# Kernel optimization log

Measured on AMD Instinct MI355X. Metric: run time of the kernel, lower is better.

Reference implementation:

```python
import jax, jax.numpy as jnp
import numpy as np

N_HEADS = 16
D_K = 64  # d_model / n_heads = 1024 / 16


def setup_inputs() -> dict:
    key = jax.random.key(0)
    ks = jax.random.split(key, 7)
    B, S, D = 4, 2048, 1024
    scale = 1.0 / np.sqrt(D)
    return {
        "Q": jax.random.normal(ks[0], (B, S, D), dtype=jnp.float32),
        "K": jax.random.normal(ks[1], (B, S, D), dtype=jnp.float32),
        "V": jax.random.normal(ks[2], (B, S, D), dtype=jnp.float32),
        # Linear weights stored as [in, out] so y = x @ W (bias=False in original).
        "WQ": jax.random.normal(ks[3], (D, D), dtype=jnp.float32) * scale,
        "WK": jax.random.normal(ks[4], (D, D), dtype=jnp.float32) * scale,
        "WV": jax.random.normal(ks[5], (D, D), dtype=jnp.float32) * scale,
        "Wfc": jax.random.normal(ks[6], (D, D), dtype=jnp.float32) * scale,
    }


def reference(Q, K, V, WQ, WK, WV, Wfc):
    B = Q.shape[0]
    # NOTE: the original uses a raw reshape [B, S, H*dk] -> [B, H, S, dk]
    # (NOT the usual view+transpose); row-major reshape reproduces it exactly.
    q = (Q @ WQ).reshape(B, N_HEADS, -1, D_K)  # [B, H, S, dk]
    k = (K @ WK).reshape(B, N_HEADS, -1, D_K)
    v = (V @ WV).reshape(B, N_HEADS, -1, D_K)
    scores = jnp.einsum("bhqd,bhkd->bhqk", q, k) / jnp.sqrt(jnp.asarray(D_K, q.dtype))
    attn = jax.nn.softmax(scores, axis=-1)
    ctx = jnp.einsum("bhqk,bhkd->bhqd", attn, v)  # [B, H, S, dk]
    ctx = jnp.transpose(ctx, (0, 2, 1, 3)).reshape(B, -1, N_HEADS * D_K)  # [B, S, D]
    return ctx @ Wfc
```

## Files before the change

### kernel.cpp

```cpp
#include <hip/hip_runtime.h>
#include <stdint.h>
#include <math.h>


typedef __attribute__((ext_vector_type(8))) short short8;
typedef __attribute__((ext_vector_type(4))) float f32x4;
typedef __attribute__((ext_vector_type(16))) float f32x16;
typedef __attribute__((ext_vector_type(2))) unsigned int u32x2;
typedef __attribute__((ext_vector_type(4))) unsigned int u32x4;
typedef __attribute__((ext_vector_type(8))) _Float16 half8;

__device__ __forceinline__ unsigned short bf16rne(float f) {
  unsigned int u = __builtin_bit_cast(unsigned int, f);
  unsigned int r = u + 0x7FFFu + ((u >> 16) & 1u);
  return (unsigned short)(r >> 16);
}

__device__ __forceinline__ void gld_lds16(const void* g, void* l) {
  typedef __attribute__((address_space(3))) unsigned int lds_u32;
  typedef const __attribute__((address_space(1))) unsigned int glb_u32;
  __builtin_amdgcn_global_load_lds((glb_u32*)(uintptr_t)g,
                                   (lds_u32*)(unsigned int)(uintptr_t)l,
                                   16, 0, 0);
}

__device__ __forceinline__ unsigned pkrtz(float a, float b) {
  auto h = __builtin_amdgcn_cvt_pkrtz(a, b);
  return __builtin_bit_cast(unsigned, h);
}

__device__ __forceinline__ float fexp2(float x) {
#if __has_builtin(__builtin_amdgcn_exp2f)
  return __builtin_amdgcn_exp2f(x);
#else
  float r;
  asm("v_exp_f32 %0, %1" : "=v"(r) : "v"(x));
  return r;
#endif
}

__device__ __forceinline__ float max3f(float a, float b, float c) {
  float r;
  asm("v_max3_f32 %0, %1, %2, %3" : "=v"(r) : "v"(a), "v"(b), "v"(c));
  return r;
}

__global__ void convert_x_kernel(const float* __restrict__ Q,
                                 const float* __restrict__ K,
                                 const float* __restrict__ V,
                                 unsigned short* __restrict__ Xb) {
  const int z = blockIdx.y;
  const float* src = (z == 0) ? Q : (z == 1) ? K : V;
  const size_t i0 = ((size_t)blockIdx.x * 256 + threadIdx.x) * 8;
  const f32x4 a = *(const f32x4*)(src + i0);
  const f32x4 c = *(const f32x4*)(src + i0 + 4);
  u32x4 o;
  o[0] = (unsigned)bf16rne(a[0]) | ((unsigned)bf16rne(a[1]) << 16);
  o[1] = (unsigned)bf16rne(a[2]) | ((unsigned)bf16rne(a[3]) << 16);
  o[2] = (unsigned)bf16rne(c[0]) | ((unsigned)bf16rne(c[1]) << 16);
  o[3] = (unsigned)bf16rne(c[2]) | ((unsigned)bf16rne(c[3]) << 16);
  *(u32x4*)(Xb + (size_t)z * 8388608 + i0) = o;
}

__global__ void convert_w_kernel(const float* __restrict__ W0,
                                 const float* __restrict__ W1,
                                 const float* __restrict__ W2,
                                 const float* __restrict__ W3,
                                 unsigned short* __restrict__ Wt) {
  const int z = blockIdx.z;
  const float* W = (z == 0) ? W0 : (z == 1) ? W1 : (z == 2) ? W2 : W3;
  unsigned short* dst = Wt + (size_t)z * 1048576;
  __shared__ float tile[32][33];
  const int tx = threadIdx.x & 31, ty = threadIdx.x >> 5;
  const int k0 = blockIdx.x * 32, n0 = blockIdx.y * 32;
#pragma unroll
  for (int yy = 0; yy < 32; yy += 8)
    tile[ty + yy][tx] = W[(size_t)(k0 + ty + yy) * 1024 + n0 + tx];
  __syncthreads();
#pragma unroll
  for (int yy = 0; yy < 32; yy += 8)
    dst[(size_t)(n0 + ty + yy) * 1024 + k0 + tx] = bf16rne(tile[tx][ty + yy]);
}

__global__ __launch_bounds__(256, 2) void gemm_bt_kernel(
    const unsigned short* __restrict__ A, const unsigned short* __restrict__ Bt,
    unsigned short* __restrict__ Cbf, float* __restrict__ Cf32, float scaleZ0) {
  constexpr int K = 1024, N = 1024;
  const int z = blockIdx.z;
  const unsigned short* Ab = A + (size_t)z * 8192 * 1024;
  const unsigned short* Bb = Bt + (size_t)z * 1024 * 1024;
  const int tid = threadIdx.x;
  const int lane = tid & 63;
  const int w = tid >> 6;
  const int l15 = lane & 15, quad = lane >> 4;
  const int rowBase = blockIdx.x * 128;
  const int colBase = blockIdx.y * 128;
  const int wrow = (w >> 1) * 64;
  const int wcol = (w & 1) * 64;
  __shared__ __align__(16) unsigned short As[128 * 64];
  __shared__ __align__(16) unsigned short Bs[128 * 64];

  const f32x4 z4 = {0.0f, 0.0f, 0.0f, 0.0f};
  f32x4 acc[4][4];
#pragma unroll
  for (int i = 0; i < 4; i++)
#pragma unroll
    for (int j = 0; j < 4; j++) acc[i][j] = z4;

  for (int k0 = 0; k0 < K; k0 += 64) {
#pragma unroll
    for (int it = 0; it < 4; it++) {
      const int slot = it * 256 + tid;
      const int row = slot >> 3;
      const int sseg = (slot & 7) ^ (row & 7);
      gld_lds16(Ab + (size_t)(rowBase + row) * K + k0 + sseg * 8,
                (void*)(As + slot * 8));
      gld_lds16(Bb + (size_t)(colBase + row) * K + k0 + sseg * 8,
                (void*)(Bs + slot * 8));
    }
    __syncthreads();
    short8 af[4][2], bfr[4][2];
#pragma unroll
    for (int i = 0; i < 4; i++) {
      const int row = wrow + i * 16 + l15;
#pragma unroll
      for (int kk = 0; kk < 2; kk++)
        af[i][kk] =
            *(const short8*)(As + (row * 8 + ((kk * 4 + quad) ^ (row & 7))) * 8);
    }
#pragma unroll
    for (int j = 0; j < 4; j++) {
      const int row = wcol + j * 16 + l15;
#pragma unroll
      for (int kk = 0; kk < 2; kk++)
        bfr[j][kk] =
            *(const short8*)(Bs + (row * 8 + ((kk * 4 + quad) ^ (row & 7))) * 8);
    }
#pragma unroll
    for (int kk = 0; kk < 2; kk++)
#pragma unroll
      for (int i = 0; i < 4; i++)
#pragma unroll
        for (int j = 0; j < 4; j++)
          acc[i][j] = __builtin_amdgcn_mfma_f32_16x16x32_bf16(
              af[i][kk], bfr[j][kk], acc[i][j], 0, 0, 0);
    __syncthreads();
  }

  const float sc = (z == 0) ? scaleZ0 : 1.0f;
#pragma unroll
  for (int i = 0; i < 4; i++) {
#pragma unroll
    for (int j = 0; j < 4; j++) {
#pragma unroll
      for (int r = 0; r < 4; r++) {
        const int row = rowBase + wrow + i * 16 + quad * 4 + r;
        const int col = colBase + wcol + j * 16 + l15;
        const float v = acc[i][j][r] * sc;
        if (Cbf != nullptr) {
          Cbf[(size_t)z * 8192 * 1024 + (size_t)row * N + col] = bf16rne(v);
        } else {
          Cf32[(size_t)row * N + col] = v;
        }
      }
    }
  }
}

__global__ void vtrans_kernel(const unsigned short* __restrict__ linv,
                              unsigned short* __restrict__ Vt) {
  const int st = blockIdx.x, bh = blockIdx.y;
  const unsigned short* vp = linv + (size_t)bh * 131072;
  __shared__ unsigned short tile[64 * 136];
  const int tid = threadIdx.x;
#pragma unroll
  for (int it = 0; it < 4; it++) {
    const int idx = it * 256 + tid;
    const int s = idx >> 3, d0 = (idx & 7) * 8;
    const u32x4 vv = *(const u32x4*)(vp + (size_t)(st * 128 + s) * 64 + d0);
#pragma unroll
    for (int m = 0; m < 4; m++) {
      const unsigned lo = vv[m] & 0xffffu, hi = vv[m] >> 16;
      const float f0 = __builtin_bit_cast(float, lo << 16);
      const float f1 = __builtin_bit_cast(float, hi << 16);
      const _Float16 h0 = (_Float16)f0, h1 = (_Float16)f1;
      tile[(d0 + 2 * m) * 136 + s] = __builtin_bit_cast(unsigned short, h0);
      tile[(d0 + 2 * m + 1) * 136 + s] = __builtin_bit_cast(unsigned short, h1);
    }
  }
  __syncthreads();
#pragma unroll
  for (int it = 0; it < 4; it++) {
    const int idx = it * 256 + tid;
    const int d = idx >> 4, s0 = (idx & 15) * 8;
    const u32x4 o = *(const u32x4*)(tile + d * 136 + s0);
    *(u32x4*)(Vt + (size_t)bh * 131072 + (size_t)d * 2048 + st * 128 + s0) = o;
  }
}

__global__ __launch_bounds__(256, 2) void attn_kernel(
    const unsigned short* __restrict__ lin, const _Float16* __restrict__ Vt,
    unsigned short* __restrict__ ctxr) {
  const int bh = blockIdx.x;
  const int qt = blockIdx.y;
  const int b = bh >> 4, h = bh & 15;
  const int tid = threadIdx.x, lane = tid & 63, w = tid >> 6;
  const int l31 = lane & 31, hl = lane >> 5, x7 = l31 & 7;
  const size_t headOff = (size_t)(b * 2048 + h * 128) * 1024;
  const unsigned short* qp = lin + headOff;
  const unsigned short* kp = lin + 8388608 + headOff;
  const _Float16* vtp = Vt + (size_t)bh * 131072;

  __shared__ __align__(16) unsigned short smem[24576];
  unsigned short(*Ks)[4096] = (unsigned short(*)[4096])smem;
  _Float16(*Vs)[4096] = (_Float16(*)[4096])(smem + 8192);
  _Float16* Pl = (_Float16*)(smem + 16384) + w * 2048;

  const int stageV = (w >= 2);
  const int wbase = (stageV ? (w - 2) : w) * 256 + lane;
  auto stage = [&](int bufn, int key0) {
#pragma unroll
    for (int i = 0; i < 4; i++) {
      const int slot = wbase + i * 64;
      const int row = slot >> 3;
      const int seg = (slot & 7) ^ (row & 7);
      if (!stageV) {
        gld_lds16(kp + (size_t)(key0 + row) * 64 + seg * 8,
                  (void*)(&Ks[bufn][slot * 8]));
      } else {
        gld_lds16(vtp + (size_t)row * 2048 + key0 + seg * 8,
                  (void*)(&Vs[bufn][slot * 8]));
      }
    }
  };

  const int qrow0 = qt * 256 + w * 64;
  short8 bq[2][4];
#pragma unroll
  for (int qg = 0; qg < 2; qg++)
#pragma unroll
    for (int ks = 0; ks < 4; ks++)
      bq[qg][ks] = *(const short8*)(qp +
                                    (size_t)(qrow0 + qg * 32 + l31) * 64 +
                                    ks * 16 + hl * 8);

  f32x16 z16;
#pragma unroll
  for (int r = 0; r < 16; r++) z16[r] = 0.0f;
  f32x16 co[2][2] = {{z16, z16}, {z16, z16}};
  float mrun[2] = {-INFINITY, -INFINITY};
  float lrun[2] = {0.0f, 0.0f};

  stage(0, 0);
  __syncthreads();

  for (int kt = 0; kt < 32; kt++) {
    const int cur = kt & 1;
    if (kt < 31) stage(cur ^ 1, (kt + 1) * 64);

    short8 kf[2][4];
#pragma unroll
    for (int g = 0; g < 2; g++)
#pragma unroll
      for (int ks = 0; ks < 4; ks++) {
        const int slot = (g * 32 + l31) * 8 + ((2 * ks + hl) ^ x7);
        kf[g][ks] = *(const short8*)(&Ks[cur][slot * 8]);
      }

    f32x16 sacc[2][2];
    __builtin_amdgcn_s_setprio(1);
#pragma unroll
    for (int qg = 0; qg < 2; qg++)
#pragma unroll
      for (int g = 0; g < 2; g++) {
        sacc[qg][g] = __builtin_amdgcn_mfma_f32_32x32x16_bf16(
            kf[g][0], bq[qg][0], z16, 0, 0, 0);
#pragma unroll
        for (int ks = 1; ks < 4; ks++)
          sacc[qg][g] = __builtin_amdgcn_mfma_f32_32x32x16_bf16(
              kf[g][ks], bq[qg][ks], sacc[qg][g], 0, 0, 0);
      }
    __builtin_amdgcn_s_setprio(0);

    half8 vf[2][2][2];
#pragma unroll
    for (int dt = 0; dt < 2; dt++)
#pragma unroll
      for (int g = 0; g < 2; g++)
#pragma unroll
        for (int s = 0; s < 2; s++) {
          const int slot = (dt * 32 + l31) * 8 + ((4 * g + 2 * s + hl) ^ x7);
          vf[dt][g][s] = *(const half8*)(&Vs[cur][slot * 8]);
        }

#pragma unroll
    for (int qg = 0; qg < 2; qg++) {
      float pmax;
      {
        float tm[8];
#pragma unroll
        for (int r = 0; r < 8; r++)
          tm[r] = fmaxf(max3f(sacc[qg][0][r], sacc[qg][0][r + 8],
                              sacc[qg][1][r]),
                        sacc[qg][1][r + 8]);
        const float a0 = max3f(tm[0], tm[1], tm[2]);
        const float a1 = max3f(tm[3], tm[4], tm[5]);
        const float a2 = fmaxf(tm[6], tm[7]);
        pmax = max3f(a0, a1, a2);
      }
      pmax = fmaxf(pmax, __shfl_xor(pmax, 32, 64));
      if (!__all(pmax - mrun[qg] <= 8.0f)) {
        const float mnew = fmaxf(mrun[qg], pmax);
        const float a = fexp2(mrun[qg] - mnew);
        mrun[qg] = mnew;
        lrun[qg] *= a;
#pragma unroll
        for (int r = 0; r < 16; r++) {
          co[qg][0][r] *= a;
          co[qg][1][r] *= a;
        }
      }
      float ls0 = 0.0f, ls1 = 0.0f, ls2 = 0.0f, ls3 = 0.0f;
#pragma unroll
      for (int g = 0; g < 2; g++) {
#pragma unroll
        for (int r = 0; r < 16; r += 4) {
          const float p0 = fexp2(sacc[qg][g][r + 0] - mrun[qg]);
          const float p1 = fexp2(sacc[qg][g][r + 1] - mrun[qg]);
          const float p2 = fexp2(sacc[qg][g][r + 2] - mrun[qg]);
          const float p3 = fexp2(sacc[qg][g][r + 3] - mrun[qg]);
          sacc[qg][g][r + 0] = p0;
          sacc[qg][g][r + 1] = p1;
          sacc[qg][g][r + 2] = p2;
          sacc[qg][g][r + 3] = p3;
          ls0 += p0;
          ls1 += p1;
          ls2 += p2;
          ls3 += p3;
        }
      }
      lrun[qg] += (ls0 + ls1) + (ls2 + ls3);

#pragma unroll
      for (int g = 0; g < 2; g++) {
#pragma unroll
        for (int rg = 0; rg < 4; rg++) {
          u32x2 pw;
          pw[0] = pkrtz(sacc[qg][g][4 * rg + 0], sacc[qg][g][4 * rg + 1]);
          pw[1] = pkrtz(sacc[qg][g][4 * rg + 2], sacc[qg][g][4 * rg + 3]);
          *(u32x2*)(Pl + l31 * 64 + (((4 * g + rg) ^ x7) * 8) + hl * 4) = pw;
        }
        half8 pf[2];
#pragma unroll
        for (int s = 0; s < 2; s++)
          pf[s] =
              *(const half8*)(Pl + l31 * 64 + (((4 * g + 2 * s + hl) ^ x7) * 8));
        __builtin_amdgcn_s_setprio(1);
#pragma unroll
        for (int dt = 0; dt < 2; dt++)
#pragma unroll
          for (int s = 0; s < 2; s++)
            co[qg][dt] = __builtin_amdgcn_mfma_f32_32x32x16_f16(
                vf[dt][g][s], pf[s], co[qg][dt], 0, 0, 0);
        __builtin_amdgcn_s_setprio(0);
      }
    }
    __syncthreads();
  }

  unsigned short* Cw = smem + w * 4608;
#pragma unroll
  for (int qg = 0; qg < 2; qg++) {
    const float l = lrun[qg] + __shfl_xor(lrun[qg], 32, 64);
    const float inv = 1.0f / l;
#pragma unroll
    for (int dt = 0; dt < 2; dt++) {
#pragma unroll
      for (int r = 0; r < 16; r++) {
        const int d = dt * 32 + (r & 3) + 8 * (r >> 2) + 4 * hl;
        Cw[(qg * 32 + l31) * 72 + d] = bf16rne(co[qg][dt][r] * inv);
      }
    }
  }
  __syncthreads();
#pragma unroll
  for (int it = 0; it < 8; it++) {
    const int q = it * 8 + (lane >> 3);
    const int seg = lane & 7;
    const u32x4 o = *(const u32x4*)(Cw + q * 72 + seg * 8);
    *(u32x4*)(ctxr + (size_t)(b * 2048 + qrow0 + q) * 1024 + h * 64 + seg * 8) = o;
  }
}

extern "C" void kernel_launch(void* const* d_in, const int* in_sizes, int n_in,
                              void* d_out, int out_size, void* d_ws, size_t ws_size,
                              hipStream_t stream) {
  const float* Q = (const float*)d_in[0];
  const float* K = (const float*)d_in[1];
  const float* V = (const float*)d_in[2];
  const float* WQ = (const float*)d_in[3];
  const float* WK = (const float*)d_in[4];
  const float* WV = (const float*)d_in[5];
  const float* Wfc = (const float*)d_in[6];
  float* out = (float*)d_out;

  unsigned short* ws = (unsigned short*)d_ws;
  unsigned short* Xb = ws;
  unsigned short* ctxr = ws;
  unsigned short* Vt = ws + 8388608;
  unsigned short* Wt = ws + 25165824;
  unsigned short* lin = ws + 29360128;

  convert_x_kernel<<<dim3(4096, 3), 256, 0, stream>>>(Q, K, V, Xb);
  convert_w_kernel<<<dim3(32, 32, 4), 256, 0, stream>>>(WQ, WK, WV, Wfc, Wt);
  const float qscale = 0.125f * 1.4426950408889634f;
  gemm_bt_kernel<<<dim3(64, 8, 3), 256, 0, stream>>>(Xb, Wt, lin, nullptr, qscale);
  vtrans_kernel<<<dim3(16, 64), 256, 0, stream>>>(lin + 16777216, Vt);
  attn_kernel<<<dim3(64, 8), 256, 0, stream>>>(lin, (const _Float16*)Vt, ctxr);
  gemm_bt_kernel<<<dim3(64, 8, 1), 256, 0, stream>>>(ctxr, Wt + 3 * 1048576, nullptr,
                                                     out, 1.0f);
}
```

Baseline: 361.5 us.

## Double-buffer LDS in projection GEMM with 256x128 tiles and 512 threads

Restructures the projection GEMM so each block computes a 256x128 tile with 8 waves instead of 128x128 with 4. The A and B tiles now sit in two LDS buffers, and the next K-step is prefetched with global_load_lds while MFMAs run on the current one, leaving one barrier per iteration. This hides global-load latency and reuses each B tile across more rows. In exchange LDS use grows to about 96KB per block, occupancy drops to one block per CU, and there are half as many blocks, so the final GEMM fills only one wave of CUs.

```diff
diff --git a/kernel.cpp b/kernel.cpp
--- a/kernel.cpp
+++ b/kernel.cpp
@@ -82,7 +82,7 @@
     dst[(size_t)(n0 + ty + yy) * 1024 + k0 + tx] = bf16rne(tile[tx][ty + yy]);
 }
 
-__global__ __launch_bounds__(256, 2) void gemm_bt_kernel(
+__global__ __launch_bounds__(512, 1) void gemm_bt_kernel(
     const unsigned short* __restrict__ A, const unsigned short* __restrict__ Bt,
     unsigned short* __restrict__ Cbf, float* __restrict__ Cf32, float scaleZ0) {
   constexpr int K = 1024, N = 1024;
@@ -93,12 +93,12 @@
   const int lane = tid & 63;
   const int w = tid >> 6;
   const int l15 = lane & 15, quad = lane >> 4;
-  const int rowBase = blockIdx.x * 128;
+  const int rowBase = blockIdx.x * 256;
   const int colBase = blockIdx.y * 128;
   const int wrow = (w >> 1) * 64;
   const int wcol = (w & 1) * 64;
-  __shared__ __align__(16) unsigned short As[128 * 64];
-  __shared__ __align__(16) unsigned short Bs[128 * 64];
+  __shared__ __align__(16) unsigned short As[2][256 * 64];
+  __shared__ __align__(16) unsigned short Bs[2][128 * 64];
 
   const f32x4 z4 = {0.0f, 0.0f, 0.0f, 0.0f};
   f32x4 acc[4][4];
@@ -107,43 +107,53 @@
 #pragma unroll
     for (int j = 0; j < 4; j++) acc[i][j] = z4;
 
-  for (int k0 = 0; k0 < K; k0 += 64) {
+  auto stage = [&](int buf, int k0) {
 #pragma unroll
     for (int it = 0; it < 4; it++) {
-      const int slot = it * 256 + tid;
+      const int slot = it * 512 + tid;
       const int row = slot >> 3;
       const int sseg = (slot & 7) ^ (row & 7);
       gld_lds16(Ab + (size_t)(rowBase + row) * K + k0 + sseg * 8,
-                (void*)(As + slot * 8));
+                (void*)(As[buf] + slot * 8));
+    }
+#pragma unroll
+    for (int it = 0; it < 2; it++) {
+      const int slot = it * 512 + tid;
+      const int row = slot >> 3;
+      const int sseg = (slot & 7) ^ (row & 7);
       gld_lds16(Bb + (size_t)(colBase + row) * K + k0 + sseg * 8,
-                (void*)(Bs + slot * 8));
-    }
-    __syncthreads();
-    short8 af[4][2], bfr[4][2];
-#pragma unroll
-    for (int i = 0; i < 4; i++) {
-      const int row = wrow + i * 16 + l15;
-#pragma unroll
-      for (int kk = 0; kk < 2; kk++)
-        af[i][kk] =
-            *(const short8*)(As + (row * 8 + ((kk * 4 + quad) ^ (row & 7))) * 8);
-    }
-#pragma unroll
-    for (int j = 0; j < 4; j++) {
-      const int row = wcol + j * 16 + l15;
-#pragma unroll
-      for (int kk = 0; kk < 2; kk++)
-        bfr[j][kk] =
-            *(const short8*)(Bs + (row * 8 + ((kk * 4 + quad) ^ (row & 7))) * 8);
-    }
-#pragma unroll
-    for (int kk = 0; kk < 2; kk++)
+                (void*)(Bs[buf] + slot * 8));
+    }
+  };
+
+  stage(0, 0);
+  __syncthreads();
+
+  for (int kt = 0; kt < K / 64; kt++) {
+    const int buf = kt & 1;
+    if (kt < K / 64 - 1) stage(buf ^ 1, (kt + 1) * 64);
+#pragma unroll
+    for (int kk = 0; kk < 2; kk++) {
+      short8 af[4], bfr[4];
+#pragma unroll
+      for (int i = 0; i < 4; i++) {
+        const int row = wrow + i * 16 + l15;
+        af[i] = *(const short8*)(As[buf] +
+                                 (row * 8 + ((kk * 4 + quad) ^ (row & 7))) * 8);
+      }
+#pragma unroll
+      for (int j = 0; j < 4; j++) {
+        const int row = wcol + j * 16 + l15;
+        bfr[j] = *(const short8*)(Bs[buf] +
+                                  (row * 8 + ((kk * 4 + quad) ^ (row & 7))) * 8);
+      }
 #pragma unroll
       for (int i = 0; i < 4; i++)
 #pragma unroll
         for (int j = 0; j < 4; j++)
           acc[i][j] = __builtin_amdgcn_mfma_f32_16x16x32_bf16(
-              af[i][kk], bfr[j][kk], acc[i][j], 0, 0, 0);
+              af[i], bfr[j], acc[i][j], 0, 0, 0);
+    }
     __syncthreads();
   }
 
@@ -414,9 +424,9 @@
   convert_x_kernel<<<dim3(4096, 3), 256, 0, stream>>>(Q, K, V, Xb);
   convert_w_kernel<<<dim3(32, 32, 4), 256, 0, stream>>>(WQ, WK, WV, Wfc, Wt);
   const float qscale = 0.125f * 1.4426950408889634f;
-  gemm_bt_kernel<<<dim3(64, 8, 3), 256, 0, stream>>>(Xb, Wt, lin, nullptr, qscale);
+  gemm_bt_kernel<<<dim3(32, 8, 3), 512, 0, stream>>>(Xb, Wt, lin, nullptr, qscale);
   vtrans_kernel<<<dim3(16, 64), 256, 0, stream>>>(lin + 16777216, Vt);
   attn_kernel<<<dim3(64, 8), 256, 0, stream>>>(lin, (const _Float16*)Vt, ctxr);
-  gemm_bt_kernel<<<dim3(64, 8, 1), 256, 0, stream>>>(ctxr, Wt + 3 * 1048576, nullptr,
+  gemm_bt_kernel<<<dim3(32, 8, 1), 512, 0, stream>>>(ctxr, Wt + 3 * 1048576, nullptr,
                                                      out, 1.0f);
 }
```

Result: faster. 348.4 us (-3.6%).
